# Kernel optimization log

Hardware: AMD Instinct MI355X
Metric: run time of the kernel (lower is better)

Reference implementation:

```python
import jax, jax.numpy as jnp
import numpy as np

N, E, FS = 50000, 400000, 256
H, D = 8, 64            # GAT heads, hidden_size (per-head out_feats)
NH, DK, DV = 8, 64, 64  # transformer MHA
B = 1024
NEG_SLOPE = 0.2
EPS = 1e-6


def _layer_norm(x, g, b, eps=EPS):
    mu = x.mean(-1, keepdims=True)
    var = x.var(-1, keepdims=True)
    return (x - mu) / jnp.sqrt(var + eps) * g + b


def setup_inputs() -> dict:
    key = jax.random.key(0)
    ks = jax.random.split(key, 20)
    s = 0.02
    return {
        "features": jax.random.normal(ks[0], (N, FS), jnp.float32),
        "src": jax.random.randint(ks[1], (E,), 0, N, jnp.int32),
        "dst": jax.random.randint(ks[2], (E,), 0, N, jnp.int32),
        "url": jax.random.randint(ks[3], (B,), 1, N + 1, jnp.int32),  # 1-based ids
        # GATConv params (DGL-style)
        "gat_fc_w": jax.random.normal(ks[4], (FS, H * D), jnp.float32) * s,
        "attn_l": jax.random.normal(ks[5], (H, D), jnp.float32) * s,
        "attn_r": jax.random.normal(ks[6], (H, D), jnp.float32) * s,
        "gat_res_w": jax.random.normal(ks[7], (FS, H * D), jnp.float32) * s,
        "gat_bias": jnp.zeros((H, D), jnp.float32),
        # post-GAT LayerNorm
        "ln_g": jnp.ones((D,), jnp.float32),
        "ln_b": jnp.zeros((D,), jnp.float32),
        # MultiHeadAttention params
        "wq": jax.random.normal(ks[8], (D, NH * DK), jnp.float32) * s,
        "wk": jax.random.normal(ks[9], (D, NH * DK), jnp.float32) * s,
        "wv": jax.random.normal(ks[10], (D, NH * DV), jnp.float32) * s,
        "fc_w": jax.random.normal(ks[11], (NH * DV, D), jnp.float32) * s,
        "fc_b": jnp.zeros((D,), jnp.float32),
        "mha_ln_g": jnp.ones((D,), jnp.float32),
        "mha_ln_b": jnp.zeros((D,), jnp.float32),
        # final classifier
        "out_w": jax.random.normal(ks[12], (D, 2), jnp.float32) * s,
        "out_b": jnp.zeros((2,), jnp.float32),
    }


def reference(features, src, dst, url, gat_fc_w, attn_l, attn_r, gat_res_w,
              gat_bias, ln_g, ln_b, wq, wk, wv, fc_w, fc_b, mha_ln_g,
              mha_ln_b, out_w, out_b):
    # ---- GATConv (residual=True, bias, negative_slope=0.2, no activation) ----
    feat = (features @ gat_fc_w).reshape(N, H, D)          # [N,H,D]
    el = jnp.einsum('nhd,hd->nh', feat, attn_l)            # [N,H]
    er = jnp.einsum('nhd,hd->nh', feat, attn_r)            # [N,H]
    e = jax.nn.leaky_relu(el[src] + er[dst], NEG_SLOPE)    # [E,H] edge scores
    # segment softmax over incoming edges of each dst node
    m = jax.ops.segment_max(e, dst, num_segments=N)        # [N,H]
    m = jnp.where(jnp.isfinite(m), m, 0.0)
    ex = jnp.exp(e - m[dst])                               # [E,H]
    denom = jax.ops.segment_sum(ex, dst, num_segments=N)   # [N,H]
    a = ex / jnp.maximum(denom[dst], 1e-20)                # [E,H]
    msg = feat[src] * a[:, :, None]                        # [E,H,D]
    rst = jax.ops.segment_sum(msg, dst, num_segments=N)    # [N,H,D]
    res = (features @ gat_res_w).reshape(N, H, D)
    gat_emb = rst + res + gat_bias                         # [N,H,D]

    # ---- select batch nodes (url is 1-based) ----
    ids = url - 1
    x = gat_emb[ids]                                       # [B,H,D]
    x = _layer_norm(x, ln_g, ln_b)

    # ---- dense multi-head self-attention over the H gat heads (seq dim) ----
    residual = x
    q = (x @ wq).reshape(B, H, NH, DK)
    k = (x @ wk).reshape(B, H, NH, DK)
    v = (x @ wv).reshape(B, H, NH, DV)
    attn = jnp.einsum('bqhd,bkhd->bhqk', q, k) / jnp.sqrt(jnp.float32(DK))
    attn = jax.nn.softmax(attn, axis=-1)
    o = jnp.einsum('bhqk,bkhd->bqhd', attn, v).reshape(B, H, NH * DV)
    o = o @ fc_w + fc_b                                    # [B,H,D]
    o = _layer_norm(o + residual, mha_ln_g, mha_ln_b)

    # ---- pool + classify ----
    pooled = o.sum(axis=1)                                 # [B,D]
    logits = pooled @ out_w + out_b                        # [B,2]
    return logits
```

## Files before the change

kernel.cpp:

```cpp
#include <hip/hip_runtime.h>
#include <math.h>

#define Nn 50000
#define Ee 400000
#define FSz 256
#define HD_ 512
#define Bb 1024
#define HSZ 2048

static __device__ __forceinline__ int clampi(int v, int lo, int hi){
    return v < lo ? lo : (v > hi ? hi : v);
}
static __device__ __forceinline__ unsigned short f2bf(float f){
    unsigned int u = __float_as_uint(f);
    unsigned int r = u + 0x7FFFu + ((u >> 16) & 1u);
    return (unsigned short)(r >> 16);
}
static __device__ __forceinline__ float bflo(unsigned int v){ return __uint_as_float(v << 16); }
static __device__ __forceinline__ float bfhi(unsigned int v){ return __uint_as_float(v & 0xFFFF0000u); }

__global__ __launch_bounds__(256) void k_scatter(const int* __restrict__ src, const int* __restrict__ dst,
                                                 const int* __restrict__ url,
                                                 int* __restrict__ fill, int* __restrict__ slist,
                                                 const float* __restrict__ W,
                                                 const float* __restrict__ al,
                                                 const float* __restrict__ ar,
                                                 float* __restrict__ wl, float* __restrict__ wr,
                                                 const float* __restrict__ Wfc,
                                                 const float* __restrict__ Wres,
                                                 unsigned int* __restrict__ wfcb,
                                                 unsigned int* __restrict__ wresb){
    int t = threadIdx.x;
    if(blockIdx.x >= 1579){
        int bi = blockIdx.x - 1579;
        int m = bi >> 4;
        const float2* Sf = (const float2*)(m ? Wres : Wfc);
        unsigned int* D = m ? wresb : wfcb;
        int base = (bi & 15) * 8192;
        #pragma unroll
        for(int i = 0; i < 32; i++){
            int idx = base + i*256 + t;
            float2 v = Sf[idx];
            D[idx] = ((unsigned int)f2bf(v.y) << 16) | (unsigned int)f2bf(v.x);
        }
        return;
    }
    if(blockIdx.x >= 1563){
        int bi = blockIdx.x - 1563;
        int wv = t >> 6, lane = t & 63;
        #pragma unroll
        for(int r = 0; r < 4; r++){
            int f = bi*16 + wv*4 + r;
            float pl[8], pr[8];
            #pragma unroll
            for(int h = 0; h < 8; h++){
                float w = W[f*512 + h*64 + lane];
                pl[h] = w * al[h*64 + lane];
                pr[h] = w * ar[h*64 + lane];
            }
            #pragma unroll
            for(int h = 0; h < 8; h++){
                #pragma unroll
                for(int m = 32; m >= 1; m >>= 1){
                    pl[h] += __shfl_xor(pl[h], m, 64);
                    pr[h] += __shfl_xor(pr[h], m, 64);
                }
            }
            #pragma unroll
            for(int h = 0; h < 8; h++){
                if(lane == h){ wl[h*256 + f] = pl[h]; wr[h*256 + f] = pr[h]; }
            }
        }
        return;
    }
    __shared__ int key[HSZ];
    __shared__ int chainhead[HSZ];
    __shared__ short nxt[Bb];
    for(int i = t; i < HSZ; i += 256){ key[i] = -1; chainhead[i] = -1; }
    __syncthreads();
    for(int b = t; b < Bb; b += 256){
        int n = clampi(url[b] - 1, 0, Nn - 1);
        int h = n & (HSZ - 1);
        while(true){
            int prev = atomicCAS(&key[h], -1, n);
            if(prev == -1 || prev == n) break;
            h = (h + 1) & (HSZ - 1);
        }
        int old = atomicExch(&chainhead[h], b);
        nxt[b] = (short)old;
    }
    __syncthreads();
    int e = blockIdx.x * 256 + t;
    if(e >= Ee) return;
    int d = dst[e];
    if((unsigned)d >= (unsigned)Nn) return;
    int h = d & (HSZ - 1);
    while(true){
        int k = key[h];
        if(k == -1) return;
        if(k == d) break;
        h = (h + 1) & (HSZ - 1);
    }
    int s = clampi(src[e], 0, Nn - 1);
    for(int b = chainhead[h]; b != -1; b = nxt[b]){
        int pos = atomicAdd(&fill[b], 1);
        if(pos < 64) slist[b*64 + pos] = s;
    }
}

__global__ __launch_bounds__(256) void k_gat(const float* __restrict__ features,
                                             const unsigned int* __restrict__ Wfcb,
                                             const unsigned int* __restrict__ Wresb,
                                             const float* __restrict__ bias,
                                             const float* __restrict__ wl,
                                             const float* __restrict__ wr,
                                             const int* __restrict__ url,
                                             const int* __restrict__ fill, const int* __restrict__ slist,
                                             float* __restrict__ gemb){
    int t = threadIdx.x;
    int lane = t & 63, wv = t >> 6;
    int u0 = blockIdx.x * 2;

    __shared__ float cxs[2][8][256];
    __shared__ float fres[2][256];
    __shared__ float sew[2][64][8];
    __shared__ float ser[2][8];
    __shared__ int   sslist[2][64];

    for(int i = t; i < 2*64*8; i += 256) ((float*)sew)[i] = 0.f;

    float4 rwl[8], rwr[8];
    #pragma unroll
    for(int h = 0; h < 8; h++){
        rwl[h] = *(const float4*)&wl[h*256 + 4*lane];
        rwr[h] = *(const float4*)&wr[h*256 + 4*lane];
    }

    int dg[2], nj[2];
    #pragma unroll
    for(int j = 0; j < 2; j++){
        int u = u0 + j;
        dg[j] = min(fill[u], 64);
        nj[j] = clampi(url[u] - 1, 0, Nn - 1);
        if(t < dg[j]) sslist[j][t] = slist[u*64 + t];
        fres[j][t] = features[(size_t)nj[j] * FSz + t];
    }
    __syncthreads();

    int c1 = dg[0];
    int total = c1 + dg[1];
    for(int tau = wv; tau < total + 2; tau += 4){
        int j, i, isEr = 0;
        if(tau < c1){ j = 0; i = tau; }
        else if(tau < total){ j = 1; i = tau - c1; }
        else { j = tau - total; i = 0; isEr = 1; }
        int s = isEr ? nj[j] : sslist[j][i];
        float4 x = *(const float4*)(features + (size_t)s * FSz + 4*lane);
        float p[8];
        if(isEr){
            #pragma unroll
            for(int h = 0; h < 8; h++)
                p[h] = x.x*rwr[h].x + x.y*rwr[h].y + x.z*rwr[h].z + x.w*rwr[h].w;
        } else {
            #pragma unroll
            for(int h = 0; h < 8; h++)
                p[h] = x.x*rwl[h].x + x.y*rwl[h].y + x.z*rwl[h].z + x.w*rwl[h].w;
        }
        #pragma unroll
        for(int h = 0; h < 8; h++){
            #pragma unroll
            for(int m = 32; m >= 1; m >>= 1) p[h] += __shfl_xor(p[h], m, 64);
        }
        if(lane == 0){
            if(isEr){
                #pragma unroll
                for(int h = 0; h < 8; h++) ser[j][h] = p[h];
            } else {
                #pragma unroll
                for(int h = 0; h < 8; h++) sew[j][i][h] = p[h];
            }
        }
    }
    __syncthreads();
    if(t < 16){
        int j = t >> 3, h = t & 7;
        int dgj = dg[j];
        if(dgj > 0){
            float ern = ser[j][h];
            float m = -1e30f;
            for(int i = 0; i < dgj; i++){
                float v = sew[j][i][h] + ern;
                v = v > 0.f ? v : 0.2f * v;
                m = fmaxf(m, v);
            }
            float sum = 0.f;
            for(int i = 0; i < dgj; i++){
                float v = sew[j][i][h] + ern;
                v = v > 0.f ? v : 0.2f * v;
                float w = expf(v - m);
                sum += w;
                sew[j][i][h] = w;
            }
            float inv = 1.0f / fmaxf(sum, 1e-20f);
            for(int i = 0; i < dgj; i++) sew[j][i][h] *= inv;
        }
    }
    __syncthreads();
    {
        float cx[2][8];
        #pragma unroll
        for(int j = 0; j < 2; j++)
            #pragma unroll
            for(int h = 0; h < 8; h++) cx[j][h] = 0.f;
        int mxd = max(dg[0], dg[1]);
        for(int i = 0; i < mxd; i += 2){
            float x[2][2];
            #pragma unroll
            for(int j = 0; j < 2; j++)
                #pragma unroll
                for(int ii = 0; ii < 2; ii++){
                    int idx = i + ii;
                    int s = (idx < dg[j]) ? sslist[j][idx] : 0;
                    x[j][ii] = features[(size_t)s * FSz + t];
                }
            #pragma unroll
            for(int j = 0; j < 2; j++)
                #pragma unroll
                for(int ii = 0; ii < 2; ii++){
                    int idx = i + ii;
                    const float* av = &sew[j][idx < 64 ? idx : 0][0];
                    float xm = (idx < dg[j]) ? x[j][ii] : 0.f;
                    #pragma unroll
                    for(int h = 0; h < 8; h++) cx[j][h] += av[h] * xm;
                }
        }
        #pragma unroll
        for(int j = 0; j < 2; j++)
            #pragma unroll
            for(int h = 0; h < 8; h++) cxs[j][h][t] = cx[j][h];
    }
    __syncthreads();

    int h = t >> 5;
    int o0 = 2 * t;
    float a[2][2] = {{0,0},{0,0}};
    for(int f = 0; f < 256; f += 4){
        unsigned int w0 = Wfcb[(f+0)*256 + t];
        unsigned int w1 = Wfcb[(f+1)*256 + t];
        unsigned int w2 = Wfcb[(f+2)*256 + t];
        unsigned int w3 = Wfcb[(f+3)*256 + t];
        unsigned int r0 = Wresb[(f+0)*256 + t];
        unsigned int r1 = Wresb[(f+1)*256 + t];
        unsigned int r2 = Wresb[(f+2)*256 + t];
        unsigned int r3 = Wresb[(f+3)*256 + t];
        #pragma unroll
        for(int j = 0; j < 2; j++){
            float4 c = *(const float4*)&cxs[j][h][f];
            float4 x = *(const float4*)&fres[j][f];
            a[j][0] += c.x*bflo(w0) + c.y*bflo(w1) + c.z*bflo(w2) + c.w*bflo(w3)
                     + x.x*bflo(r0) + x.y*bflo(r1) + x.z*bflo(r2) + x.w*bflo(r3);
            a[j][1] += c.x*bfhi(w0) + c.y*bfhi(w1) + c.z*bfhi(w2) + c.w*bfhi(w3)
                     + x.x*bfhi(r0) + x.y*bfhi(r1) + x.z*bfhi(r2) + x.w*bfhi(r3);
        }
    }
    float b0 = bias[o0], b1 = bias[o0 + 1];
    #pragma unroll
    for(int j = 0; j < 2; j++){
        float2* gp = (float2*)(gemb + (size_t)(u0 + j) * HD_);
        gp[t] = make_float2(a[j][0] + b0, a[j][1] + b1);
    }
}

__global__ __launch_bounds__(256, 2) void k_mha(const float* __restrict__ gemb,
                                             const float* __restrict__ lng, const float* __restrict__ lnb,
                                             const float* __restrict__ wq, const float* __restrict__ wk,
                                             const float* __restrict__ wvp, const float* __restrict__ fcw,
                                             const float* __restrict__ fcb, const float* __restrict__ mlg,
                                             const float* __restrict__ mlb, const float* __restrict__ outw,
                                             const float* __restrict__ outb, float* __restrict__ out){
    __shared__ float A[2][512];
    __shared__ float xnF[2][512];
    __shared__ unsigned short xnT[2][512];
    __shared__ unsigned short qkb[2][8320];
    __shared__ float mu8[2][8], rs8[2][8], pooled[2][64];

    int t = threadIdx.x;
    int lane = t & 63, wv = t >> 6;
    int e0 = blockIdx.x * 2;

    {
        const float* g0 = gemb + (size_t)e0 * HD_;
        const float* g1 = gemb + (size_t)(e0 + 1) * HD_;
        A[0][t] = g0[t]; A[0][t + 256] = g0[t + 256];
        A[1][t] = g1[t]; A[1][t + 256] = g1[t + 256];
    }
    __syncthreads();
    if(t < 16){
        int ee = t >> 3, q = t & 7;
        float s = 0.f, s2 = 0.f;
        for(int d = 0; d < 64; d++){ float v = A[ee][q*64 + d]; s += v; s2 += v * v; }
        float mu = s * (1.0f/64.0f);
        float var = s2 * (1.0f/64.0f) - mu * mu;
        mu8[ee][q] = mu; rs8[ee][q] = rsqrtf(fmaxf(var, 0.0f) + 1e-6f);
    }
    __syncthreads();
    #pragma unroll
    for(int p = 0; p < 4; p++){
        int i = p*256 + t; int ee = i >> 9, ii = i & 511, q = ii >> 6, d = ii & 63;
        float xv = (A[ee][ii] - mu8[ee][q]) * rs8[ee][q] * lng[d] + lnb[d];
        xnF[ee][ii] = xv;
        xnT[ee][d*8 + q] = f2bf(xv);
    }
    __syncthreads();
    float aq0[2][8], aq1[2][8], ak0[2][8], ak1[2][8], av0[2][8], av1[2][8];
    #pragma unroll
    for(int ee = 0; ee < 2; ee++)
        #pragma unroll
        for(int r = 0; r < 8; r++){
            aq0[ee][r]=0.f; aq1[ee][r]=0.f; ak0[ee][r]=0.f;
            ak1[ee][r]=0.f; av0[ee][r]=0.f; av1[ee][r]=0.f;
        }
    #pragma unroll 2
    for(int d = 0; d < 64; d++){
        float q0 = wq[d*512 + t],  q1 = wq[d*512 + t + 256];
        float k0 = wk[d*512 + t],  k1 = wk[d*512 + t + 256];
        float v0 = wvp[d*512 + t], v1 = wvp[d*512 + t + 256];
        #pragma unroll
        for(int ee = 0; ee < 2; ee++){
            uint4 xp = *(const uint4*)&xnT[ee][d*8];
            float xv[8] = { bflo(xp.x), bfhi(xp.x), bflo(xp.y), bfhi(xp.y),
                            bflo(xp.z), bfhi(xp.z), bflo(xp.w), bfhi(xp.w) };
            #pragma unroll
            for(int r = 0; r < 8; r++){
                aq0[ee][r] += xv[r]*q0; aq1[ee][r] += xv[r]*q1;
                ak0[ee][r] += xv[r]*k0; ak1[ee][r] += xv[r]*k1;
                av0[ee][r] += xv[r]*v0; av1[ee][r] += xv[r]*v1;
            }
        }
    }
    #pragma unroll
    for(int ee = 0; ee < 2; ee++)
        #pragma unroll
        for(int qq = 0; qq < 8; qq++){
            qkb[ee][qq*520 + t]              = f2bf(aq0[ee][qq]);
            qkb[ee][qq*520 + t + 256]        = f2bf(aq1[ee][qq]);
            qkb[ee][4160 + qq*520 + t]       = f2bf(ak0[ee][qq]);
            qkb[ee][4160 + qq*520 + t + 256] = f2bf(ak1[ee][qq]);
        }
    __syncthreads();
    #pragma unroll
    for(int p = 0; p < 4; p++){
        int i = p*256 + t;
        int ee = i >> 9, idx = i & 511;
        int nh = idx >> 6, qq = (idx >> 3) & 7, kk = idx & 7;
        const unsigned short* qrow = &qkb[ee][qq*520 + nh*64];
        const unsigned short* krow = &qkb[ee][4160 + kk*520 + nh*64];
        float s = 0.f;
        #pragma unroll
        for(int d8 = 0; d8 < 64; d8 += 8){
            uint4 qv = *(const uint4*)&qrow[d8];
            uint4 kv = *(const uint4*)&krow[d8];
            s += bflo(qv.x)*bflo(kv.x) + bfhi(qv.x)*bfhi(kv.x)
               + bflo(qv.y)*bflo(kv.y) + bfhi(qv.y)*bfhi(kv.y)
               + bflo(qv.z)*bflo(kv.z) + bfhi(qv.z)*bfhi(kv.z)
               + bflo(qv.w)*bflo(kv.w) + bfhi(qv.w)*bfhi(kv.w);
        }
        A[ee][idx] = s * 0.125f;
    }
    __syncthreads();
    if(t < 128){
        int ee = t >> 6, row = t & 63;
        float mx = -1e30f;
        #pragma unroll
        for(int k = 0; k < 8; k++) mx = fmaxf(mx, A[ee][row*8 + k]);
        float e[8]; float s = 0.f;
        #pragma unroll
        for(int k = 0; k < 8; k++){ e[k] = expf(A[ee][row*8 + k] - mx); s += e[k]; }
        float inv = 1.0f / s;
        #pragma unroll
        for(int k = 0; k < 8; k++) A[ee][row*8 + k] = e[k] * inv;
    }
    __syncthreads();
    {
        int nh0 = wv;
        #pragma unroll
        for(int ee = 0; ee < 2; ee++){
            #pragma unroll
            for(int qq = 0; qq < 8; qq++){
                const float* s0 = &A[ee][nh0*64 + qq*8];
                const float* s1 = &A[ee][(nh0+4)*64 + qq*8];
                float4 a0 = *(const float4*)s0, b0 = *(const float4*)(s0 + 4);
                float4 a1 = *(const float4*)s1, b1 = *(const float4*)(s1 + 4);
                float o0 = a0.x*av0[ee][0] + a0.y*av0[ee][1] + a0.z*av0[ee][2] + a0.w*av0[ee][3]
                         + b0.x*av0[ee][4] + b0.y*av0[ee][5] + b0.z*av0[ee][6] + b0.w*av0[ee][7];
                float o1 = a1.x*av1[ee][0] + a1.y*av1[ee][1] + a1.z*av1[ee][2] + a1.w*av1[ee][3]
                         + b1.x*av1[ee][4] + b1.y*av1[ee][5] + b1.z*av1[ee][6] + b1.w*av1[ee][7];
                qkb[ee][qq*520 + t]       = f2bf(o0);
                qkb[ee][qq*520 + t + 256] = f2bf(o1);
            }
        }
    }
    __syncthreads();
    {
        float* P0 = (float*)&qkb[0][4160];
        float* P1 = (float*)&qkb[1][4160];
        int g = lane & 31;
        int qh = lane >> 5;
        int k0r = wv * 128;
        float a[2][4][2];
        #pragma unroll
        for(int ee = 0; ee < 2; ee++)
            #pragma unroll
            for(int jq = 0; jq < 4; jq++){ a[ee][jq][0] = 0.f; a[ee][jq][1] = 0.f; }
        const float2* fw2 = (const float2*)fcw;
        for(int k = k0r; k < k0r + 128; k += 8){
            float2 f0 = fw2[(k+0)*32 + g];
            float2 f1 = fw2[(k+1)*32 + g];
            float2 f2 = fw2[(k+2)*32 + g];
            float2 f3 = fw2[(k+3)*32 + g];
            float2 f4 = fw2[(k+4)*32 + g];
            float2 f5 = fw2[(k+5)*32 + g];
            float2 f6 = fw2[(k+6)*32 + g];
            float2 f7 = fw2[(k+7)*32 + g];
            #pragma unroll
            for(int ee = 0; ee < 2; ee++){
                #pragma unroll
                for(int jq = 0; jq < 4; jq++){
                    int qq = qh*4 + jq;
                    uint4 op = *(const uint4*)&qkb[ee][qq*520 + k];
                    float x0 = bflo(op.x), x1 = bfhi(op.x), x2 = bflo(op.y), x3 = bfhi(op.y);
                    float x4 = bflo(op.z), x5 = bfhi(op.z), x6 = bflo(op.w), x7 = bfhi(op.w);
                    a[ee][jq][0] += x0*f0.x + x1*f1.x + x2*f2.x + x3*f3.x + x4*f4.x + x5*f5.x + x6*f6.x + x7*f7.x;
                    a[ee][jq][1] += x0*f0.y + x1*f1.y + x2*f2.y + x3*f3.y + x4*f4.y + x5*f5.y + x6*f6.y + x7*f7.y;
                }
            }
        }
        __syncthreads();
        #pragma unroll
        for(int jq = 0; jq < 4; jq++){
            int qq = qh*4 + jq;
            *(float2*)&P0[wv*512 + qq*64 + 2*g] = make_float2(a[0][jq][0], a[0][jq][1]);
            *(float2*)&P1[wv*512 + qq*64 + 2*g] = make_float2(a[1][jq][0], a[1][jq][1]);
        }
        __syncthreads();
        #pragma unroll
        for(int p = 0; p < 4; p++){
            int i = p*256 + t;
            int ee = i >> 9, o = i & 511, dd = o & 63;
            const float* P = ee ? P1 : P0;
            A[ee][o] = P[o] + P[512 + o] + P[1024 + o] + P[1536 + o] + fcb[dd] + xnF[ee][o];
        }
    }
    __syncthreads();
    if(t < 16){
        int ee = t >> 3, q = t & 7;
        float s = 0.f, s2 = 0.f;
        for(int d = 0; d < 64; d++){ float v = A[ee][q*64 + d]; s += v; s2 += v * v; }
        float mu = s * (1.0f/64.0f);
        float var = s2 * (1.0f/64.0f) - mu * mu;
        mu8[ee][q] = mu; rs8[ee][q] = rsqrtf(fmaxf(var, 0.0f) + 1e-6f);
    }
    __syncthreads();
    if(t < 128){
        int ee = t >> 6, dd = t & 63;
        float g2 = mlg[dd], bb = mlb[dd];
        float s = 0.f;
        #pragma unroll
        for(int qq = 0; qq < 8; qq++)
            s += (A[ee][qq*64 + dd] - mu8[ee][qq]) * rs8[ee][qq] * g2 + bb;
        pooled[ee][dd] = s;
    }
    __syncthreads();
    if(t < 4){
        int ee = t >> 1, c = t & 1;
        float s = outb[c];
        for(int d = 0; d < 64; d++) s += pooled[ee][d] * outw[d*2 + c];
        out[(e0 + ee)*2 + c] = s;
    }
}

extern "C" void kernel_launch(void* const* d_in, const int* in_sizes, int n_in,
                              void* d_out, int out_size, void* d_ws, size_t ws_size,
                              hipStream_t stream){
    (void)in_sizes; (void)n_in; (void)out_size; (void)ws_size;
    const float* features  = (const float*)d_in[0];
    const int*   src       = (const int*)d_in[1];
    const int*   dst       = (const int*)d_in[2];
    const int*   url       = (const int*)d_in[3];
    const float* gat_fc_w  = (const float*)d_in[4];
    const float* attn_l    = (const float*)d_in[5];
    const float* attn_r    = (const float*)d_in[6];
    const float* gat_res_w = (const float*)d_in[7];
    const float* gat_bias  = (const float*)d_in[8];
    const float* ln_g      = (const float*)d_in[9];
    const float* ln_b      = (const float*)d_in[10];
    const float* wq        = (const float*)d_in[11];
    const float* wk        = (const float*)d_in[12];
    const float* wv        = (const float*)d_in[13];
    const float* fc_w      = (const float*)d_in[14];
    const float* fc_b      = (const float*)d_in[15];
    const float* mha_ln_g  = (const float*)d_in[16];
    const float* mha_ln_b  = (const float*)d_in[17];
    const float* out_w     = (const float*)d_in[18];
    const float* out_b     = (const float*)d_in[19];

    char* base = (char*)d_ws;
    size_t cur = 0;
    auto alloc = [&](size_t nbytes) -> void* {
        void* p = base + cur;
        cur = (cur + nbytes + 255) & ~(size_t)255;
        return p;
    };
    float*        wl    = (float*)alloc(2048 * sizeof(float));
    float*        wr    = (float*)alloc(2048 * sizeof(float));
    int*          fill  = (int*)alloc(1024 * sizeof(int));
    int*          slist = (int*)alloc((size_t)1024 * 64 * sizeof(int));
    float*        gemb  = (float*)alloc((size_t)1024 * 512 * sizeof(float));
    unsigned int* wfcb  = (unsigned int*)alloc((size_t)256 * 512 * sizeof(unsigned short));
    unsigned int* wresb = (unsigned int*)alloc((size_t)256 * 512 * sizeof(unsigned short));

    hipMemsetAsync(fill, 0, 1024 * sizeof(int), stream);

    hipLaunchKernelGGL(k_scatter, dim3(1611), dim3(256), 0, stream, src, dst, url, fill, slist,
                       gat_fc_w, attn_l, attn_r, wl, wr, gat_fc_w, gat_res_w, wfcb, wresb);
    hipLaunchKernelGGL(k_gat,     dim3(512),  dim3(256), 0, stream, features, wfcb, wresb, gat_bias,
                       wl, wr, url, fill, slist, gemb);
    hipLaunchKernelGGL(k_mha,     dim3(512),  dim3(256), 0, stream, gemb, ln_g, ln_b,
                       wq, wk, wv, fc_w, fc_b, mha_ln_g, mha_ln_b, out_w, out_b,
                       (float*)d_out);
}
```

Before: 199.6 us.

## Process one batch row per MHA block and parallelize layernorm and classifier reductions

The MHA kernel now handles one batch element per block instead of two, doubling the grid to 1024 blocks and halving shared memory and register accumulators, with launch bounds raised to 4 blocks per SM. Layernorm statistics are computed by 64 threads with wavefront shuffles instead of 16 serial threads, and the final classifier dot product uses a shuffle reduction. The aim is more parallelism and occupancy plus shorter serial tails. In exchange, each weight row loaded for the QKV and fc projections is reused for only one batch row, so global/L2 weight traffic doubles.

```diff
diff --git a/kernel.cpp b/kernel.cpp
--- a/kernel.cpp
+++ b/kernel.cpp
@@ -271,90 +271,85 @@
     }
 }
 
-__global__ __launch_bounds__(256, 2) void k_mha(const float* __restrict__ gemb,
+__global__ __launch_bounds__(256, 4) void k_mha(const float* __restrict__ gemb,
                                              const float* __restrict__ lng, const float* __restrict__ lnb,
                                              const float* __restrict__ wq, const float* __restrict__ wk,
                                              const float* __restrict__ wvp, const float* __restrict__ fcw,
                                              const float* __restrict__ fcb, const float* __restrict__ mlg,
                                              const float* __restrict__ mlb, const float* __restrict__ outw,
                                              const float* __restrict__ outb, float* __restrict__ out){
-    __shared__ float A[2][512];
-    __shared__ float xnF[2][512];
-    __shared__ unsigned short xnT[2][512];
-    __shared__ unsigned short qkb[2][8320];
-    __shared__ float mu8[2][8], rs8[2][8], pooled[2][64];
+    __shared__ float A[512];
+    __shared__ float xnF[512];
+    __shared__ unsigned short xnT[512];
+    __shared__ unsigned short qkb[8320];
+    __shared__ float mu8[8], rs8[8], pooled[64];
 
     int t = threadIdx.x;
-    int lane = t & 63, wv = t >> 6;
-    int e0 = blockIdx.x * 2;
+    int wv = t >> 6;
+    int e = blockIdx.x;
 
     {
-        const float* g0 = gemb + (size_t)e0 * HD_;
-        const float* g1 = gemb + (size_t)(e0 + 1) * HD_;
-        A[0][t] = g0[t]; A[0][t + 256] = g0[t + 256];
-        A[1][t] = g1[t]; A[1][t + 256] = g1[t + 256];
-    }
-    __syncthreads();
-    if(t < 16){
-        int ee = t >> 3, q = t & 7;
+        const float* g0 = gemb + (size_t)e * HD_;
+        A[t] = g0[t]; A[t + 256] = g0[t + 256];
+    }
+    __syncthreads();
+    if(t < 64){
+        int q = t >> 3, d0 = t & 7;
         float s = 0.f, s2 = 0.f;
-        for(int d = 0; d < 64; d++){ float v = A[ee][q*64 + d]; s += v; s2 += v * v; }
-        float mu = s * (1.0f/64.0f);
-        float var = s2 * (1.0f/64.0f) - mu * mu;
-        mu8[ee][q] = mu; rs8[ee][q] = rsqrtf(fmaxf(var, 0.0f) + 1e-6f);
-    }
-    __syncthreads();
-    #pragma unroll
-    for(int p = 0; p < 4; p++){
-        int i = p*256 + t; int ee = i >> 9, ii = i & 511, q = ii >> 6, d = ii & 63;
-        float xv = (A[ee][ii] - mu8[ee][q]) * rs8[ee][q] * lng[d] + lnb[d];
-        xnF[ee][ii] = xv;
-        xnT[ee][d*8 + q] = f2bf(xv);
-    }
-    __syncthreads();
-    float aq0[2][8], aq1[2][8], ak0[2][8], ak1[2][8], av0[2][8], av1[2][8];
-    #pragma unroll
-    for(int ee = 0; ee < 2; ee++)
-        #pragma unroll
-        for(int r = 0; r < 8; r++){
-            aq0[ee][r]=0.f; aq1[ee][r]=0.f; ak0[ee][r]=0.f;
-            ak1[ee][r]=0.f; av0[ee][r]=0.f; av1[ee][r]=0.f;
-        }
+        #pragma unroll
+        for(int k = 0; k < 8; k++){ float v = A[q*64 + d0 + 8*k]; s += v; s2 += v * v; }
+        #pragma unroll
+        for(int m = 1; m <= 4; m <<= 1){ s += __shfl_xor(s, m, 64); s2 += __shfl_xor(s2, m, 64); }
+        if(d0 == 0){
+            float mu = s * (1.0f/64.0f);
+            float var = s2 * (1.0f/64.0f) - mu * mu;
+            mu8[q] = mu; rs8[q] = rsqrtf(fmaxf(var, 0.0f) + 1e-6f);
+        }
+    }
+    __syncthreads();
+    #pragma unroll
+    for(int p = 0; p < 2; p++){
+        int i = p*256 + t; int q = i >> 6, d = i & 63;
+        float xv = (A[i] - mu8[q]) * rs8[q] * lng[d] + lnb[d];
+        xnF[i] = xv;
+        xnT[d*8 + q] = f2bf(xv);
+    }
+    __syncthreads();
+    float aq0[8], aq1[8], ak0[8], ak1[8], av0[8], av1[8];
+    #pragma unroll
+    for(int r = 0; r < 8; r++){
+        aq0[r]=0.f; aq1[r]=0.f; ak0[r]=0.f;
+        ak1[r]=0.f; av0[r]=0.f; av1[r]=0.f;
+    }
     #pragma unroll 2
     for(int d = 0; d < 64; d++){
         float q0 = wq[d*512 + t],  q1 = wq[d*512 + t + 256];
         float k0 = wk[d*512 + t],  k1 = wk[d*512 + t + 256];
         float v0 = wvp[d*512 + t], v1 = wvp[d*512 + t + 256];
-        #pragma unroll
-        for(int ee = 0; ee < 2; ee++){
-            uint4 xp = *(const uint4*)&xnT[ee][d*8];
-            float xv[8] = { bflo(xp.x), bfhi(xp.x), bflo(xp.y), bfhi(xp.y),
-                            bflo(xp.z), bfhi(xp.z), bflo(xp.w), bfhi(xp.w) };
-            #pragma unroll
-            for(int r = 0; r < 8; r++){
-                aq0[ee][r] += xv[r]*q0; aq1[ee][r] += xv[r]*q1;
-                ak0[ee][r] += xv[r]*k0; ak1[ee][r] += xv[r]*k1;
-                av0[ee][r] += xv[r]*v0; av1[ee][r] += xv[r]*v1;
-            }
-        }
-    }
-    #pragma unroll
-    for(int ee = 0; ee < 2; ee++)
-        #pragma unroll
-        for(int qq = 0; qq < 8; qq++){
-            qkb[ee][qq*520 + t]              = f2bf(aq0[ee][qq]);
-            qkb[ee][qq*520 + t + 256]        = f2bf(aq1[ee][qq]);
-            qkb[ee][4160 + qq*520 + t]       = f2bf(ak0[ee][qq]);
-            qkb[ee][4160 + qq*520 + t + 256] = f2bf(ak1[ee][qq]);
-        }
-    __syncthreads();
-    #pragma unroll
-    for(int p = 0; p < 4; p++){
-        int i = p*256 + t;
-        int ee = i >> 9, idx = i & 511;
+        uint4 xp = *(const uint4*)&xnT[d*8];
+        float xv[8] = { bflo(xp.x), bfhi(xp.x), bflo(xp.y), bfhi(xp.y),
+                        bflo(xp.z), bfhi(xp.z), bflo(xp.w), bfhi(xp.w) };
+        #pragma unroll
+        for(int r = 0; r < 8; r++){
+            aq0[r] += xv[r]*q0; aq1[r] += xv[r]*q1;
+            ak0[r] += xv[r]*k0; ak1[r] += xv[r]*k1;
+            av0[r] += xv[r]*v0; av1[r] += xv[r]*v1;
+        }
+    }
+    #pragma unroll
+    for(int qq = 0; qq < 8; qq++){
+        qkb[qq*520 + t]              = f2bf(aq0[qq]);
+        qkb[qq*520 + t + 256]        = f2bf(aq1[qq]);
+        qkb[4160 + qq*520 + t]       = f2bf(ak0[qq]);
+        qkb[4160 + qq*520 + t + 256] = f2bf(ak1[qq]);
+    }
+    __syncthreads();
+    #pragma unroll
+    for(int p = 0; p < 2; p++){
+        int idx = p*256 + t;
         int nh = idx >> 6, qq = (idx >> 3) & 7, kk = idx & 7;
-        const unsigned short* qrow = &qkb[ee][qq*520 + nh*64];
-        const unsigned short* krow = &qkb[ee][4160 + kk*520 + nh*64];
+        const unsigned short* qrow = &qkb[qq*520 + nh*64];
+        const unsigned short* krow = &qkb[4160 + kk*520 + nh*64];
         float s = 0.f;
         #pragma unroll
         for(int d8 = 0; d8 < 64; d8 += 8){
@@ -365,53 +360,47 @@
                + bflo(qv.z)*bflo(kv.z) + bfhi(qv.z)*bfhi(kv.z)
                + bflo(qv.w)*bflo(kv.w) + bfhi(qv.w)*bfhi(kv.w);
         }
-        A[ee][idx] = s * 0.125f;
-    }
-    __syncthreads();
-    if(t < 128){
-        int ee = t >> 6, row = t & 63;
+        A[idx] = s * 0.125f;
+    }
+    __syncthreads();
+    if(t < 64){
+        int row = t;
         float mx = -1e30f;
         #pragma unroll
-        for(int k = 0; k < 8; k++) mx = fmaxf(mx, A[ee][row*8 + k]);
-        float e[8]; float s = 0.f;
-        #pragma unroll
-        for(int k = 0; k < 8; k++){ e[k] = expf(A[ee][row*8 + k] - mx); s += e[k]; }
+        for(int k = 0; k < 8; k++) mx = fmaxf(mx, A[row*8 + k]);
+        float ev[8]; float s = 0.f;
+        #pragma unroll
+        for(int k = 0; k < 8; k++){ ev[k] = expf(A[row*8 + k] - mx); s += ev[k]; }
         float inv = 1.0f / s;
         #pragma unroll
-        for(int k = 0; k < 8; k++) A[ee][row*8 + k] = e[k] * inv;
+        for(int k = 0; k < 8; k++) A[row*8 + k] = ev[k] * inv;
     }
     __syncthreads();
     {
         int nh0 = wv;
         #pragma unroll
-        for(int ee = 0; ee < 2; ee++){
-            #pragma unroll
-            for(int qq = 0; qq < 8; qq++){
-                const float* s0 = &A[ee][nh0*64 + qq*8];
-                const float* s1 = &A[ee][(nh0+4)*64 + qq*8];
-                float4 a0 = *(const float4*)s0, b0 = *(const float4*)(s0 + 4);
-                float4 a1 = *(const float4*)s1, b1 = *(const float4*)(s1 + 4);
-                float o0 = a0.x*av0[ee][0] + a0.y*av0[ee][1] + a0.z*av0[ee][2] + a0.w*av0[ee][3]
-                         + b0.x*av0[ee][4] + b0.y*av0[ee][5] + b0.z*av0[ee][6] + b0.w*av0[ee][7];
-                float o1 = a1.x*av1[ee][0] + a1.y*av1[ee][1] + a1.z*av1[ee][2] + a1.w*av1[ee][3]
-                         + b1.x*av1[ee][4] + b1.y*av1[ee][5] + b1.z*av1[ee][6] + b1.w*av1[ee][7];
-                qkb[ee][qq*520 + t]       = f2bf(o0);
-                qkb[ee][qq*520 + t + 256] = f2bf(o1);
-            }
+        for(int qq = 0; qq < 8; qq++){
+            const float* s0 = &A[nh0*64 + qq*8];
+            const float* s1 = &A[(nh0+4)*64 + qq*8];
+            float4 a0 = *(const float4*)s0, b0 = *(const float4*)(s0 + 4);
+            float4 a1 = *(const float4*)s1, b1 = *(const float4*)(s1 + 4);
+            float o0 = a0.x*av0[0] + a0.y*av0[1] + a0.z*av0[2] + a0.w*av0[3]
+                     + b0.x*av0[4] + b0.y*av0[5] + b0.z*av0[6] + b0.w*av0[7];
+            float o1 = a1.x*av1[0] + a1.y*av1[1] + a1.z*av1[2] + a1.w*av1[3]
+                     + b1.x*av1[4] + b1.y*av1[5] + b1.z*av1[6] + b1.w*av1[7];
+            qkb[qq*520 + t]       = f2bf(o0);
+            qkb[qq*520 + t + 256] = f2bf(o1);
         }
     }
     __syncthreads();
     {
-        float* P0 = (float*)&qkb[0][4160];
-        float* P1 = (float*)&qkb[1][4160];
-        int g = lane & 31;
-        int qh = lane >> 5;
+        float* P = (float*)&qkb[4160];
+        int g = (t & 63) & 31;
+        int qh = (t & 63) >> 5;
         int k0r = wv * 128;
-        float a[2][4][2];
-        #pragma unroll
-        for(int ee = 0; ee < 2; ee++)
-            #pragma unroll
-            for(int jq = 0; jq < 4; jq++){ a[ee][jq][0] = 0.f; a[ee][jq][1] = 0.f; }
+        float a[4][2];
+        #pragma unroll
+        for(int jq = 0; jq < 4; jq++){ a[jq][0] = 0.f; a[jq][1] = 0.f; }
         const float2* fw2 = (const float2*)fcw;
         for(int k = k0r; k < k0r + 128; k += 8){
             float2 f0 = fw2[(k+0)*32 + g];
@@ -423,59 +412,59 @@
             float2 f6 = fw2[(k+6)*32 + g];
             float2 f7 = fw2[(k+7)*32 + g];
             #pragma unroll
-            for(int ee = 0; ee < 2; ee++){
-                #pragma unroll
-                for(int jq = 0; jq < 4; jq++){
-                    int qq = qh*4 + jq;
-                    uint4 op = *(const uint4*)&qkb[ee][qq*520 + k];
-                    float x0 = bflo(op.x), x1 = bfhi(op.x), x2 = bflo(op.y), x3 = bfhi(op.y);
-                    float x4 = bflo(op.z), x5 = bfhi(op.z), x6 = bflo(op.w), x7 = bfhi(op.w);
-                    a[ee][jq][0] += x0*f0.x + x1*f1.x + x2*f2.x + x3*f3.x + x4*f4.x + x5*f5.x + x6*f6.x + x7*f7.x;
-                    a[ee][jq][1] += x0*f0.y + x1*f1.y + x2*f2.y + x3*f3.y + x4*f4.y + x5*f5.y + x6*f6.y + x7*f7.y;
-                }
+            for(int jq = 0; jq < 4; jq++){
+                int qq = qh*4 + jq;
+                uint4 op = *(const uint4*)&qkb[qq*520 + k];
+                float x0 = bflo(op.x), x1 = bfhi(op.x), x2 = bflo(op.y), x3 = bfhi(op.y);
+                float x4 = bflo(op.z), x5 = bfhi(op.z), x6 = bflo(op.w), x7 = bfhi(op.w);
+                a[jq][0] += x0*f0.x + x1*f1.x + x2*f2.x + x3*f3.x + x4*f4.x + x5*f5.x + x6*f6.x + x7*f7.x;
+                a[jq][1] += x0*f0.y + x1*f1.y + x2*f2.y + x3*f3.y + x4*f4.y + x5*f5.y + x6*f6.y + x7*f7.y;
             }
         }
         __syncthreads();
         #pragma unroll
         for(int jq = 0; jq < 4; jq++){
             int qq = qh*4 + jq;
-            *(float2*)&P0[wv*512 + qq*64 + 2*g] = make_float2(a[0][jq][0], a[0][jq][1]);
-            *(float2*)&P1[wv*512 + qq*64 + 2*g] = make_float2(a[1][jq][0], a[1][jq][1]);
+            *(float2*)&P[wv*512 + qq*64 + 2*g] = make_float2(a[jq][0], a[jq][1]);
         }
         __syncthreads();
         #pragma unroll
-        for(int p = 0; p < 4; p++){
-            int i = p*256 + t;
-            int ee = i >> 9, o = i & 511, dd = o & 63;
-            const float* P = ee ? P1 : P0;
-            A[ee][o] = P[o] + P[512 + o] + P[1024 + o] + P[1536 + o] + fcb[dd] + xnF[ee][o];
-        }
-    }
-    __syncthreads();
-    if(t < 16){
-        int ee = t >> 3, q = t & 7;
+        for(int p = 0; p < 2; p++){
+            int o = p*256 + t; int dd = o & 63;
+            A[o] = P[o] + P[512 + o] + P[1024 + o] + P[1536 + o] + fcb[dd] + xnF[o];
+        }
+    }
+    __syncthreads();
+    if(t < 64){
+        int q = t >> 3, d0 = t & 7;
         float s = 0.f, s2 = 0.f;
-        for(int d = 0; d < 64; d++){ float v = A[ee][q*64 + d]; s += v; s2 += v * v; }
-        float mu = s * (1.0f/64.0f);
-        float var = s2 * (1.0f/64.0f) - mu * mu;
-        mu8[ee][q] = mu; rs8[ee][q] = rsqrtf(fmaxf(var, 0.0f) + 1e-6f);
-    }
-    __syncthreads();
-    if(t < 128){
-        int ee = t >> 6, dd = t & 63;
+        #pragma unroll
+        for(int k = 0; k < 8; k++){ float v = A[q*64 + d0 + 8*k]; s += v; s2 += v * v; }
+        #pragma unroll
+        for(int m = 1; m <= 4; m <<= 1){ s += __shfl_xor(s, m, 64); s2 += __shfl_xor(s2, m, 64); }
+        if(d0 == 0){
+            float mu = s * (1.0f/64.0f);
+            float var = s2 * (1.0f/64.0f) - mu * mu;
+            mu8[q] = mu; rs8[q] = rsqrtf(fmaxf(var, 0.0f) + 1e-6f);
+        }
+    }
+    __syncthreads();
+    if(t < 64){
+        int dd = t;
         float g2 = mlg[dd], bb = mlb[dd];
         float s = 0.f;
         #pragma unroll
         for(int qq = 0; qq < 8; qq++)
-            s += (A[ee][qq*64 + dd] - mu8[ee][qq]) * rs8[ee][qq] * g2 + bb;
-        pooled[ee][dd] = s;
-    }
-    __syncthreads();
-    if(t < 4){
-        int ee = t >> 1, c = t & 1;
-        float s = outb[c];
-        for(int d = 0; d < 64; d++) s += pooled[ee][d] * outw[d*2 + c];
-        out[(e0 + ee)*2 + c] = s;
+            s += (A[qq*64 + dd] - mu8[qq]) * rs8[qq] * g2 + bb;
+        pooled[dd] = s;
+    }
+    __syncthreads();
+    if(t < 128){
+        int c = t >> 6, d = t & 63;
+        float v = pooled[d] * outw[d*2 + c];
+        #pragma unroll
+        for(int m = 32; m >= 1; m >>= 1) v += __shfl_xor(v, m, 64);
+        if((t & 63) == 0) out[e*2 + c] = v + outb[c];
     }
 }
 
@@ -525,7 +514,7 @@
                        gat_fc_w, attn_l, attn_r, wl, wr, gat_fc_w, gat_res_w, wfcb, wresb);
     hipLaunchKernelGGL(k_gat,     dim3(512),  dim3(256), 0, stream, features, wfcb, wresb, gat_bias,
                        wl, wr, url, fill, slist, gemb);
-    hipLaunchKernelGGL(k_mha,     dim3(512),  dim3(256), 0, stream, gemb, ln_g, ln_b,
+    hipLaunchKernelGGL(k_mha,     dim3(1024), dim3(256), 0, stream, gemb, ln_g, ln_b,
                        wq, wk, wv, fc_w, fc_b, mha_ln_g, mha_ln_b, out_w, out_b,
                        (float*)d_out);
 }
```

Result: slower. 208.0 us (+4.2%).
